# Kernel tuning notes

Measured on AMD Instinct MI355X. Metric: run time of the kernel, lower is better.

Reference implementation:

```python
import jax, jax.numpy as jnp
import numpy as np

T, D, N, K, H = 4096, 2560, 8, 4, 256
QUERY_PRE_ATTN_SCALAR = 256.0
ROPE_THETA = 10000.0
RMS_EPS = 1e-6
SLIDING_WINDOW = 1024
NEG_INF = -1e30


def setup_inputs() -> dict:
    key = jax.random.key(0)
    ks = jax.random.split(key, 6)
    return {
        "x": jax.random.normal(ks[0], (T, D), dtype=jnp.float32),
        "wq": jax.random.normal(ks[1], (D, N, H), dtype=jnp.float32) * 0.02,
        "wk": jax.random.normal(ks[2], (D, K, H), dtype=jnp.float32) * 0.02,
        "wv": jax.random.normal(ks[3], (D, K, H), dtype=jnp.float32) * 0.02,
        "wo": jax.random.normal(ks[4], (N, H, D), dtype=jnp.float32) * 0.02,
        "q_norm_w": jnp.ones((H,), dtype=jnp.float32),
        "k_norm_w": jnp.ones((H,), dtype=jnp.float32),
        "positions": jnp.arange(T, dtype=jnp.int32),
    }


def rms_norm(x, w, eps=RMS_EPS):
    rms = jnp.sqrt(jnp.mean(x * x, axis=-1, keepdims=True) + eps)
    return w * (x / rms)


def apply_rope(x, positions, head_dim, theta):
    # x: [T, heads, H]; rotate-half RoPE
    half = head_dim // 2
    inv_freq = theta ** (-(jnp.arange(half, dtype=jnp.float32) * 2.0 / head_dim))
    ang = positions.astype(jnp.float32)[:, None] * inv_freq  # [T, half]
    sin = jnp.sin(ang)[:, None, :]
    cos = jnp.cos(ang)[:, None, :]
    x1, x2 = jnp.split(x, 2, axis=-1)
    return jnp.concatenate([x1 * cos - x2 * sin, x2 * cos + x1 * sin], axis=-1)


def reference(x, wq, wk, wv, wo, q_norm_w, k_norm_w, positions):
    # QKV projections (per-head)
    q = jnp.einsum('td,dnh->tnh', x, wq)            # [T, N, H]
    q = rms_norm(q, q_norm_w)
    q = q * (QUERY_PRE_ATTN_SCALAR ** -0.5)
    q = apply_rope(q, positions, H, ROPE_THETA)

    k = jnp.einsum('td,dkh->tkh', x, wk)            # [T, K, H]
    k = rms_norm(k, k_norm_w)
    k = apply_rope(k, positions, H, ROPE_THETA)

    v = jnp.einsum('td,dkh->tkh', x, wv)            # [T, K, H]

    # GQA sliding-window causal attention
    G = N // K
    qh = q.reshape(T, K, G, H)
    scores = jnp.einsum('tkgh,skh->kgts', qh, k)    # [K, G, T, T]
    pq = positions[:, None]
    pk = positions[None, :]
    mask = (pk <= pq) & (pq - pk < SLIDING_WINDOW)  # [T, T]
    scores = jnp.where(mask, scores, NEG_INF)
    p = jax.nn.softmax(scores, axis=-1)
    attn = jnp.einsum('kgts,skh->tkgh', p, v).reshape(T, N, H)

    o = jnp.einsum('tnh,nhd->td', attn, wo)         # [T, D]
    new_kv_cache = jnp.stack([k, v])                # [2, T, K, H]
    return new_kv_cache, o
```

## Files before the change

kernel.cpp:

```cpp
#include <hip/hip_runtime.h>
#include <stdint.h>

#define T_TOK 4096
#define DM    2560
#define NQ    8
#define NKV   4
#define HD    256
#define WIN   1024

using bf16x8 = __attribute__((ext_vector_type(8))) short;
using f32x4  = __attribute__((ext_vector_type(4))) float;
typedef unsigned short u16;

__device__ __forceinline__ u16 f2bf(float x) {
  union { float f; uint32_t u; } v; v.f = x;
  uint32_t u = v.u;
  return (u16)((u + 0x7fffu + ((u >> 16) & 1u)) >> 16);
}
__device__ __forceinline__ float bf2f(u16 b) {
  union { uint32_t u; float f; } v; v.u = ((uint32_t)b) << 16;
  return v.f;
}

__device__ __forceinline__ void async_cp16(const void* g, void* lds) {
  __builtin_amdgcn_global_load_lds(
      (const __attribute__((address_space(1))) uint32_t*)(uintptr_t)g,
      (__attribute__((address_space(3))) uint32_t*)(uint32_t)(uintptr_t)lds,
      16, 0, 0);
}

__global__ __launch_bounds__(256) void convert_f32_bf16(
    const float* __restrict__ in, u16* __restrict__ out, int n)
{
  for (int i = (blockIdx.x * 256 + threadIdx.x) * 4; i < n; i += gridDim.x * 256 * 4) {
    float4 v = *(const float4*)(in + i);
    ushort4 o;
    o.x = f2bf(v.x); o.y = f2bf(v.y); o.z = f2bf(v.z); o.w = f2bf(v.w);
    *(ushort4*)(out + i) = o;
  }
}

__global__ __launch_bounds__(256) void transpose_f32_bf16(
    const float* __restrict__ in, u16* __restrict__ out, int R, int C)
{
  __shared__ u16 tile[64][65];
  const int r0 = blockIdx.y * 64, c0 = blockIdx.x * 64;
  const int tr = threadIdx.x >> 6, tc = threadIdx.x & 63;
  #pragma unroll
  for (int i = 0; i < 16; ++i) {
    int r = tr + i * 4;
    tile[r][tc] = f2bf(in[(size_t)(r0 + r) * C + c0 + tc]);
  }
  __syncthreads();
  #pragma unroll
  for (int i = 0; i < 16; ++i) {
    int c = tr + i * 4;
    out[(size_t)(c0 + c) * R + r0 + tc] = tile[tc][c];
  }
}

template<bool F32OUT>
__global__ __launch_bounds__(512, 2) void gemm256(
    const u16* __restrict__ A, const u16* __restrict__ B, void* __restrict__ Cv,
    int Kd, int lda, int ldb, int ldc)
{
  __shared__ __align__(16) u16 lds[2][2][256 * 64];
  const int tid = threadIdx.x;
  const int wave = tid >> 6, lane = tid & 63;
  const int lg = lane >> 4, lc = lane & 15;
  const int wr = wave >> 2, wc = wave & 3;
  const int nwg = gridDim.x, bid = blockIdx.x;
  const int nid = (bid & 7) * (nwg >> 3) + (bid >> 3);
  const int m0 = (nid & 15) * 256, n0 = (nid >> 4) * 256;
  const int NT = Kd >> 6;

  const int srow = tid >> 3;
  const int scol = ((tid & 7) * 16) ^ ((srow & 7) << 4);
  const u16* Ag = A + (size_t)(m0 + srow) * lda + (scol >> 1);
  const u16* Bg = B + (size_t)(n0 + srow) * ldb + (scol >> 1);
  char* ldsA0 = (char*)&lds[0][0][0];
  char* ldsB0 = (char*)&lds[0][1][0];
  char* ldsA1 = (char*)&lds[1][0][0];
  char* ldsB1 = (char*)&lds[1][1][0];

  #define STAGE256(LA, LB, KT) do {                                         \
    const int kc_ = (KT) * 64;                                              \
    _Pragma("unroll")                                                       \
    for (int li = 0; li < 4; ++li)                                          \
      async_cp16(Ag + (size_t)(li * 64) * lda + kc_, (LA) + li * 8192 + wave * 1024); \
    _Pragma("unroll")                                                       \
    for (int li = 0; li < 4; ++li)                                          \
      async_cp16(Bg + (size_t)(li * 64) * ldb + kc_, (LB) + li * 8192 + wave * 1024); \
  } while (0)

  const f32x4 zf = {0.f, 0.f, 0.f, 0.f};
  f32x4 acc[8][4];
  #pragma unroll
  for (int i = 0; i < 8; ++i)
    #pragma unroll
    for (int j = 0; j < 4; ++j) acc[i][j] = zf;

  STAGE256(ldsA0, ldsB0, 0);
  STAGE256(ldsA1, ldsB1, 1);
  asm volatile("s_waitcnt vmcnt(8)" ::: "memory");
  __builtin_amdgcn_s_barrier();
  __builtin_amdgcn_sched_barrier(0);

  for (int t = 0; t < NT; ++t) {
    const int cur = t & 1;
    const u16* Ab = &lds[cur][0][0];
    const u16* Bb = &lds[cur][1][0];

    bf16x8 bf[4][2];
    #pragma unroll
    for (int j = 0; j < 4; ++j)
      #pragma unroll
      for (int k2 = 0; k2 < 2; ++k2) {
        const int row = wc * 64 + j * 16 + lc;
        const int cb = k2 * 64 + lg * 16;
        bf[j][k2] = *(const bf16x8*)((const char*)Bb + row * 128 + (cb ^ ((row & 7) << 4)));
      }

    #pragma unroll
    for (int p = 0; p < 4; ++p) {
      bf16x8 af[2][2];
      #pragma unroll
      for (int im = 0; im < 2; ++im)
        #pragma unroll
        for (int k2 = 0; k2 < 2; ++k2) {
          const int row = wr * 128 + (p * 2 + im) * 16 + lc;
          const int cb = k2 * 64 + lg * 16;
          af[im][k2] = *(const bf16x8*)((const char*)Ab + row * 128 + (cb ^ ((row & 7) << 4)));
        }
      __builtin_amdgcn_s_setprio(1);
      #pragma unroll
      for (int im = 0; im < 2; ++im)
        #pragma unroll
        for (int j = 0; j < 4; ++j)
          #pragma unroll
          for (int k2 = 0; k2 < 2; ++k2)
            acc[p * 2 + im][j] = __builtin_amdgcn_mfma_f32_16x16x32_bf16(
                af[im][k2], bf[j][k2], acc[p * 2 + im][j], 0, 0, 0);
      __builtin_amdgcn_s_setprio(0);
    }

    __builtin_amdgcn_s_barrier();
    __builtin_amdgcn_sched_barrier(0);
    int nk = t + 2; if (nk > NT - 1) nk = NT - 1;
    if (cur == 0) { STAGE256(ldsA0, ldsB0, nk); } else { STAGE256(ldsA1, ldsB1, nk); }
    asm volatile("s_waitcnt vmcnt(8)" ::: "memory");
    __builtin_amdgcn_s_barrier();
    __builtin_amdgcn_sched_barrier(0);
  }
  #undef STAGE256

  #pragma unroll
  for (int i = 0; i < 8; ++i)
    #pragma unroll
    for (int j = 0; j < 4; ++j)
      #pragma unroll
      for (int r = 0; r < 4; ++r) {
        const int row = m0 + wr * 128 + i * 16 + lg * 4 + r;
        const int col = n0 + wc * 64 + j * 16 + lc;
        if (F32OUT) ((float*)Cv)[(size_t)row * ldc + col] = acc[i][j][r];
        else        ((u16*)Cv)[(size_t)row * ldc + col] = f2bf(acc[i][j][r]);
      }
}

__global__ __launch_bounds__(256) void fuse_norm_rope(
    const u16* __restrict__ qkv, const float* __restrict__ qnw, const float* __restrict__ knw,
    const int* __restrict__ pos, u16* __restrict__ qb, u16* __restrict__ kb,
    u16* __restrict__ vb, float* __restrict__ kvout)
{
  const int t = blockIdx.x;
  const int wave = threadIdx.x >> 6, lane = threadIdx.x & 63;
  const float p = (float)pos[t];
  const float kf = 0.10381025296523007f;
  float s0, c0, s1, c1;
  sincosf(p * exp2f(-(float)lane * kf), &s0, &c0);
  sincosf(p * exp2f(-(float)(lane + 64) * kf), &s1, &c1);
  const u16* row = qkv + (size_t)t * 4096;

  for (int pp = 0; pp < 4; ++pp) {
    const int hr = pp * 4 + wave;
    if (hr >= 12) {
      const int kk = hr - 12;
      const u16* src = row + 3072 + kk * 256;
      float* dstf = kvout + (size_t)T_TOK * NKV * HD + ((size_t)t * NKV + kk) * HD;
      u16*   dstb = vb + ((size_t)t * NKV + kk) * HD;
      #pragma unroll
      for (int q4 = 0; q4 < 4; ++q4) {
        const u16 s = src[lane + q4 * 64];
        dstf[lane + q4 * 64] = bf2f(s);
        dstb[lane + q4 * 64] = s;
      }
    } else {
      const bool isq = hr < 8;
      const int cb = isq ? hr * 256 : 2048 + (hr - 8) * 256;
      float v0 = bf2f(row[cb + lane]);
      float v1 = bf2f(row[cb + lane + 64]);
      float v2 = bf2f(row[cb + lane + 128]);
      float v3 = bf2f(row[cb + lane + 192]);
      float ss = v0 * v0 + v1 * v1 + v2 * v2 + v3 * v3;
      #pragma unroll
      for (int off = 1; off < 64; off <<= 1) ss += __shfl_xor(ss, off);
      float sc = rsqrtf(ss * (1.0f / 256.0f) + 1e-6f);
      if (isq) sc *= 0.0625f;
      const float* wn = isq ? qnw : knw;
      v0 *= sc * wn[lane];
      v1 *= sc * wn[lane + 64];
      v2 *= sc * wn[lane + 128];
      v3 *= sc * wn[lane + 192];
      const float n0 = v0 * c0 - v2 * s0;
      const float n2 = v2 * c0 + v0 * s0;
      const float n1 = v1 * c1 - v3 * s1;
      const float n3 = v3 * c1 + v1 * s1;
      if (isq) {
        u16* dst = qb + (size_t)t * 2048 + hr * 256;
        dst[lane]       = f2bf(n0);
        dst[lane + 64]  = f2bf(n1);
        dst[lane + 128] = f2bf(n2);
        dst[lane + 192] = f2bf(n3);
      } else {
        const int kk = hr - 8;
        float* dstf = kvout + ((size_t)t * NKV + kk) * HD;
        dstf[lane]       = n0;
        dstf[lane + 64]  = n1;
        dstf[lane + 128] = n2;
        dstf[lane + 192] = n3;
        u16* dstb = kb + ((size_t)t * NKV + kk) * HD;
        dstb[lane]       = f2bf(n0);
        dstb[lane + 64]  = f2bf(n1);
        dstb[lane + 128] = f2bf(n2);
        dstb[lane + 192] = f2bf(n3);
      }
    }
  }
}

__global__ __launch_bounds__(256) void transpose_v(
    const u16* __restrict__ vc, u16* __restrict__ vt)
{
  __shared__ u16 tile[64][65];
  const int kk = blockIdx.z;
  const int t0 = blockIdx.y * 64, h0 = blockIdx.x * 64;
  const int tr = threadIdx.x >> 6, tc = threadIdx.x & 63;
  #pragma unroll
  for (int i = 0; i < 16; ++i) {
    int tt = tr + i * 4;
    tile[tt][tc] = vc[((size_t)(t0 + tt) * NKV + kk) * HD + h0 + tc];
  }
  __syncthreads();
  #pragma unroll
  for (int i = 0; i < 16; ++i) {
    int h = tr + i * 4;
    vt[(size_t)kk * HD * T_TOK + (size_t)(h0 + h) * T_TOK + t0 + tc] = tile[tc][h];
  }
}

__global__ __launch_bounds__(256, 2) void attn_kernel(
    const u16* __restrict__ qb, const u16* __restrict__ kc,
    const u16* __restrict__ vt, u16* __restrict__ ob)
{
  __shared__ __align__(16) u16 Ks[64 * 256];
  __shared__ __align__(16) u16 Vts[256 * 64];
  __shared__ __align__(16) u16 Ps[4][16 * 64];

  const int n = blockIdx.y, kk = n >> 1;
  const int t0 = blockIdx.x * 64;
  const int tid = threadIdx.x;
  const int wave = tid >> 6, lane = tid & 63;
  const int lg = lane >> 4, lc = lane & 15;
  const int lswz = (lc & 7) << 4;
  const f32x4 zf = {0.f, 0.f, 0.f, 0.f};

  const int lrowK = wave * 2 + (lane >> 5);
  const int scolK = ((lane & 31) * 16) ^ ((lrowK & 7) << 4);
  const int lrowV = wave * 8 + (lane >> 3);
  const int scolV = ((lane & 7) * 16) ^ ((lrowV & 7) << 4);

  bf16x8 qf[8];
  {
    const u16* qp = qb + (size_t)(t0 + wave * 16 + lc) * 2048 + n * 256 + lg * 8;
    #pragma unroll
    for (int ks = 0; ks < 8; ++ks) qf[ks] = *(const bf16x8*)(qp + ks * 32);
  }

  f32x4 o_acc[16];
  #pragma unroll
  for (int j = 0; j < 16; ++j) o_acc[j] = zf;
  float m_r[4], l_r[4];
  #pragma unroll
  for (int r = 0; r < 4; ++r) { m_r[r] = -1e30f; l_r[r] = 0.f; }

  const int mtile = t0 >> 6;
  const int ktf = (mtile >= 16) ? (mtile - 16) : 0;

  for (int kt = ktf; kt <= mtile; ++kt) {
    const int kb = kt * 64;
    {
      const u16* kp = kc + (size_t)(kb + lrowK) * (NKV * HD) + kk * HD + (scolK >> 1);
      #pragma unroll
      for (int is = 0; is < 8; ++is)
        async_cp16(kp + (size_t)(is * 8) * (NKV * HD), (char*)Ks + is * 4096 + wave * 1024);
      const u16* vp = vt + (size_t)kk * (HD * T_TOK) + (size_t)lrowV * T_TOK + kb + (scolV >> 1);
      #pragma unroll
      for (int is = 0; is < 8; ++is)
        async_cp16(vp + (size_t)(is * 32) * T_TOK, (char*)Vts + is * 4096 + wave * 1024);
    }
    __syncthreads();

    f32x4 sf[4];
    #pragma unroll
    for (int j = 0; j < 4; ++j) sf[j] = zf;
    __builtin_amdgcn_s_setprio(1);
    #pragma unroll
    for (int ks = 0; ks < 8; ++ks)
      #pragma unroll
      for (int j = 0; j < 4; ++j) {
        const int row = j * 16 + lc;
        bf16x8 kf = *(const bf16x8*)((char*)Ks + ((row * 512 + ks * 64 + lg * 16) ^ lswz));
        sf[j] = __builtin_amdgcn_mfma_f32_16x16x32_bf16(qf[ks], kf, sf[j], 0, 0, 0);
      }
    __builtin_amdgcn_s_setprio(0);

    const bool interior = (kb >= t0 - 960) && (kb <= t0 - 64);
    if (!interior) {
      #pragma unroll
      for (int j = 0; j < 4; ++j) {
        const int gcol = kb + j * 16 + lc;
        #pragma unroll
        for (int r = 0; r < 4; ++r) {
          const int grow = t0 + wave * 16 + lg * 4 + r;
          if ((unsigned)(grow - gcol) >= WIN) sf[j][r] = -1e30f;
        }
      }
    }

    float a_r[4];
    #pragma unroll
    for (int r = 0; r < 4; ++r) {
      float v = fmaxf(fmaxf(sf[0][r], sf[1][r]), fmaxf(sf[2][r], sf[3][r]));
      v = fmaxf(v, __shfl_xor(v, 1));
      v = fmaxf(v, __shfl_xor(v, 2));
      v = fmaxf(v, __shfl_xor(v, 4));
      v = fmaxf(v, __shfl_xor(v, 8));
      const float mn = fmaxf(m_r[r], v);
      a_r[r] = __expf(m_r[r] - mn);
      m_r[r] = mn;
    }

    char* myP = (char*)&Ps[wave][0];
    #pragma unroll
    for (int r = 0; r < 4; ++r) {
      const int row = lg * 4 + r;
      const int rsw = (row & 7) << 4;
      float su = 0.f;
      #pragma unroll
      for (int j = 0; j < 4; ++j) {
        const float p = __expf(sf[j][r] - m_r[r]);
        su += p;
        *(u16*)(myP + ((row * 128 + (j * 16 + lc) * 2) ^ rsw)) = f2bf(p);
      }
      su += __shfl_xor(su, 1);
      su += __shfl_xor(su, 2);
      su += __shfl_xor(su, 4);
      su += __shfl_xor(su, 8);
      l_r[r] = l_r[r] * a_r[r] + su;
    }

    #pragma unroll
    for (int j = 0; j < 16; ++j) {
      o_acc[j][0] *= a_r[0];
      o_acc[j][1] *= a_r[1];
      o_acc[j][2] *= a_r[2];
      o_acc[j][3] *= a_r[3];
    }

    bf16x8 pa[2];
    #pragma unroll
    for (int ks = 0; ks < 2; ++ks)
      pa[ks] = *(const bf16x8*)(myP + ((lc * 128 + ks * 64 + lg * 16) ^ lswz));
    __builtin_amdgcn_s_setprio(1);
    #pragma unroll
    for (int ks = 0; ks < 2; ++ks)
      #pragma unroll
      for (int j = 0; j < 16; ++j) {
        const int row = j * 16 + lc;
        bf16x8 vf = *(const bf16x8*)((char*)Vts + ((row * 128 + ks * 64 + lg * 16) ^ lswz));
        o_acc[j] = __builtin_amdgcn_mfma_f32_16x16x32_bf16(pa[ks], vf, o_acc[j], 0, 0, 0);
      }
    __builtin_amdgcn_s_setprio(0);
    __syncthreads();
  }

  #pragma unroll
  for (int r = 0; r < 4; ++r) {
    const float li = 1.f / l_r[r];
    const size_t rowb = (size_t)(t0 + wave * 16 + lg * 4 + r) * 2048 + n * 256 + lc;
    #pragma unroll
    for (int j = 0; j < 16; ++j)
      ob[rowb + j * 16] = f2bf(o_acc[j][r] * li);
  }
}

extern "C" void kernel_launch(void* const* d_in, const int* in_sizes, int n_in,
                              void* d_out, int out_size, void* d_ws, size_t ws_size,
                              hipStream_t stream)
{
  (void)in_sizes; (void)n_in; (void)out_size; (void)ws_size;
  const float* x   = (const float*)d_in[0];
  const float* wq  = (const float*)d_in[1];
  const float* wk  = (const float*)d_in[2];
  const float* wv  = (const float*)d_in[3];
  const float* wo  = (const float*)d_in[4];
  const float* qnw = (const float*)d_in[5];
  const float* knw = (const float*)d_in[6];
  const int*   pos = (const int*)d_in[7];
  float* out = (float*)d_out;

  char* ws = (char*)d_ws;
  u16* woT   = (u16*)(ws);
  u16* xb    = (u16*)(ws + 10485760);
  u16* wqkvT = (u16*)(ws + 31457280);
  u16* qkv   = (u16*)(ws + 52428800);
  u16* q_b   = xb;
  u16* kb    = wqkvT;
  u16* vb    = (u16*)(ws + 31457280 + 8388608);
  u16* vtb   = qkv;
  u16* attn  = (u16*)(ws + 52428800 + 8388608);

  convert_f32_bf16<<<2048, 256, 0, stream>>>(x, xb, T_TOK * DM);
  transpose_f32_bf16<<<dim3(32, 40), 256, 0, stream>>>(wq, wqkvT, DM, 2048);
  transpose_f32_bf16<<<dim3(16, 40), 256, 0, stream>>>(wk, wqkvT + 2048 * DM, DM, 1024);
  transpose_f32_bf16<<<dim3(16, 40), 256, 0, stream>>>(wv, wqkvT + 3072 * DM, DM, 1024);
  transpose_f32_bf16<<<dim3(40, 32), 256, 0, stream>>>(wo, woT, 2048, DM);

  gemm256<false><<<256, 512, 0, stream>>>(xb, wqkvT, qkv, DM, DM, DM, 4096);

  fuse_norm_rope<<<T_TOK, 256, 0, stream>>>(qkv, qnw, knw, pos, q_b, kb, vb, out);

  transpose_v<<<dim3(4, 64, 4), 256, 0, stream>>>(vb, vtb);

  attn_kernel<<<dim3(64, 8), 256, 0, stream>>>(q_b, kb, vtb, attn);

  gemm256<true><<<160, 512, 0, stream>>>(attn, woT, out + 2 * (size_t)T_TOK * NKV * HD,
                                         2048, 2048, 2048, DM);
}
```

Before: 269.8 us.

## Share K/V tiles across GQA head pair and double-buffer K/V staging

The attention kernel now runs one 512-thread block per KV group and query tile. Eight waves cover both query heads of the group, so each K/V tile is loaded into LDS once instead of twice. K/V staging is double-buffered: the next tile's async copies are issued before computing on the current one, so load latency overlaps with MFMA work. LDS use roughly doubles to about 144KB per block and the grid halves to 256 blocks, which limits residency to one block per CU.

```diff
diff --git a/kernel.cpp b/kernel.cpp
--- a/kernel.cpp
+++ b/kernel.cpp
@@ -258,30 +258,46 @@
   }
 }
 
-__global__ __launch_bounds__(256, 2) void attn_kernel(
+__global__ __launch_bounds__(512, 1) void attn_kernel(
     const u16* __restrict__ qb, const u16* __restrict__ kc,
     const u16* __restrict__ vt, u16* __restrict__ ob)
 {
-  __shared__ __align__(16) u16 Ks[64 * 256];
-  __shared__ __align__(16) u16 Vts[256 * 64];
-  __shared__ __align__(16) u16 Ps[4][16 * 64];
-
-  const int n = blockIdx.y, kk = n >> 1;
+  __shared__ __align__(16) u16 Ks[2][64 * 256];
+  __shared__ __align__(16) u16 Vts[2][256 * 64];
+  __shared__ __align__(16) u16 Ps[8][16 * 64];
+
+  const int kk = blockIdx.y;
   const int t0 = blockIdx.x * 64;
   const int tid = threadIdx.x;
   const int wave = tid >> 6, lane = tid & 63;
   const int lg = lane >> 4, lc = lane & 15;
+  const int hq = kk * 2 + (wave >> 2);
+  const int wrow = (wave & 3) * 16;
   const int lswz = (lc & 7) << 4;
   const f32x4 zf = {0.f, 0.f, 0.f, 0.f};
 
-  const int lrowK = wave * 2 + (lane >> 5);
-  const int scolK = ((lane & 31) * 16) ^ ((lrowK & 7) << 4);
-  const int lrowV = wave * 8 + (lane >> 3);
-  const int scolV = ((lane & 7) * 16) ^ ((lrowV & 7) << 4);
+  const int lrowK = tid >> 5;
+  const int scolK = ((tid & 31) * 16) ^ ((lrowK & 7) << 4);
+  const int lrowV = tid >> 3;
+  const int scolV = ((tid & 7) * 16) ^ ((lrowV & 7) << 4);
+
+  #define STAGEKV(KT, BUF) do {                                                \
+    const int kb_ = (KT) * 64;                                                 \
+    const u16* kp_ = kc + (size_t)(kb_ + lrowK) * (NKV * HD) + kk * HD + (scolK >> 1); \
+    _Pragma("unroll")                                                          \
+    for (int is = 0; is < 4; ++is)                                             \
+      async_cp16(kp_ + (size_t)(is * 16) * (NKV * HD),                         \
+                 (char*)&Ks[BUF][0] + is * 8192 + wave * 1024);                \
+    const u16* vp_ = vt + (size_t)kk * (HD * T_TOK) + (size_t)lrowV * T_TOK + kb_ + (scolV >> 1); \
+    _Pragma("unroll")                                                          \
+    for (int is = 0; is < 4; ++is)                                             \
+      async_cp16(vp_ + (size_t)(is * 64) * T_TOK,                              \
+                 (char*)&Vts[BUF][0] + is * 8192 + wave * 1024);               \
+  } while (0)
 
   bf16x8 qf[8];
   {
-    const u16* qp = qb + (size_t)(t0 + wave * 16 + lc) * 2048 + n * 256 + lg * 8;
+    const u16* qp = qb + (size_t)(t0 + wrow + lc) * 2048 + hq * 256 + lg * 8;
     #pragma unroll
     for (int ks = 0; ks < 8; ++ks) qf[ks] = *(const bf16x8*)(qp + ks * 32);
   }
@@ -296,19 +312,16 @@
   const int mtile = t0 >> 6;
   const int ktf = (mtile >= 16) ? (mtile - 16) : 0;
 
+  STAGEKV(ktf, 0);
+  __syncthreads();
+
+  int cur = 0;
   for (int kt = ktf; kt <= mtile; ++kt) {
     const int kb = kt * 64;
-    {
-      const u16* kp = kc + (size_t)(kb + lrowK) * (NKV * HD) + kk * HD + (scolK >> 1);
-      #pragma unroll
-      for (int is = 0; is < 8; ++is)
-        async_cp16(kp + (size_t)(is * 8) * (NKV * HD), (char*)Ks + is * 4096 + wave * 1024);
-      const u16* vp = vt + (size_t)kk * (HD * T_TOK) + (size_t)lrowV * T_TOK + kb + (scolV >> 1);
-      #pragma unroll
-      for (int is = 0; is < 8; ++is)
-        async_cp16(vp + (size_t)(is * 32) * T_TOK, (char*)Vts + is * 4096 + wave * 1024);
-    }
-    __syncthreads();
+    if (kt < mtile) STAGEKV(kt + 1, cur ^ 1);
+
+    const u16* Kb = &Ks[cur][0];
+    const u16* Vb = &Vts[cur][0];
 
     f32x4 sf[4];
     #pragma unroll
@@ -319,7 +332,7 @@
       #pragma unroll
       for (int j = 0; j < 4; ++j) {
         const int row = j * 16 + lc;
-        bf16x8 kf = *(const bf16x8*)((char*)Ks + ((row * 512 + ks * 64 + lg * 16) ^ lswz));
+        bf16x8 kf = *(const bf16x8*)((const char*)Kb + ((row * 512 + ks * 64 + lg * 16) ^ lswz));
         sf[j] = __builtin_amdgcn_mfma_f32_16x16x32_bf16(qf[ks], kf, sf[j], 0, 0, 0);
       }
     __builtin_amdgcn_s_setprio(0);
@@ -331,7 +344,7 @@
         const int gcol = kb + j * 16 + lc;
         #pragma unroll
         for (int r = 0; r < 4; ++r) {
-          const int grow = t0 + wave * 16 + lg * 4 + r;
+          const int grow = t0 + wrow + lg * 4 + r;
           if ((unsigned)(grow - gcol) >= WIN) sf[j][r] = -1e30f;
         }
       }
@@ -387,17 +400,20 @@
       #pragma unroll
       for (int j = 0; j < 16; ++j) {
         const int row = j * 16 + lc;
-        bf16x8 vf = *(const bf16x8*)((char*)Vts + ((row * 128 + ks * 64 + lg * 16) ^ lswz));
+        bf16x8 vf = *(const bf16x8*)((const char*)Vb + ((row * 128 + ks * 64 + lg * 16) ^ lswz));
         o_acc[j] = __builtin_amdgcn_mfma_f32_16x16x32_bf16(pa[ks], vf, o_acc[j], 0, 0, 0);
       }
     __builtin_amdgcn_s_setprio(0);
+
     __syncthreads();
-  }
+    cur ^= 1;
+  }
+  #undef STAGEKV
 
   #pragma unroll
   for (int r = 0; r < 4; ++r) {
     const float li = 1.f / l_r[r];
-    const size_t rowb = (size_t)(t0 + wave * 16 + lg * 4 + r) * 2048 + n * 256 + lc;
+    const size_t rowb = (size_t)(t0 + wrow + lg * 4 + r) * 2048 + hq * 256 + lc;
     #pragma unroll
     for (int j = 0; j < 16; ++j)
       ob[rowb + j * 16] = f2bf(o_acc[j][r] * li);
@@ -442,7 +458,7 @@
 
   transpose_v<<<dim3(4, 64, 4), 256, 0, stream>>>(vb, vtb);
 
-  attn_kernel<<<dim3(64, 8), 256, 0, stream>>>(q_b, kb, vtb, attn);
+  attn_kernel<<<dim3(64, 4), 512, 0, stream>>>(q_b, kb, vtb, attn);
 
   gemm256<true><<<160, 512, 0, stream>>>(attn, woT, out + 2 * (size_t)T_TOK * NKV * HD,
                                          2048, 2048, 2048, DM);
```

New measurement: 268.2 us. About the same (-0.6%).
